# Kernel optimization log

Measured on AMD Instinct MI355X. Metric: run time of the kernel, lower is better.

## Reference

```python
import jax, jax.numpy as jnp
import numpy as np

NUM_FIELDS = 40
EMBED_DIM = 128
BATCH = 1024
NUM_IX = NUM_FIELDS * (NUM_FIELDS - 1) // 2  # 780


def _pair_indices(num_fields):
    row, col = [], []
    for i in range(num_fields - 1):
        for j in range(i + 1, num_fields):
            row.append(i)
            col.append(j)
    return np.asarray(row, dtype=np.int32), np.asarray(col, dtype=np.int32)


def setup_inputs() -> dict:
    key = jax.random.key(0)
    k1, k2 = jax.random.split(key)
    x = jax.random.normal(k1, (BATCH, NUM_FIELDS, EMBED_DIM), dtype=jnp.float32)
    # 'mat' kernel: (embed_dim, num_ix, embed_dim), random_normal init
    kernel = jax.random.normal(k2, (EMBED_DIM, NUM_IX, EMBED_DIM), dtype=jnp.float32) * 0.05
    return {"x": x, "kernel": kernel}


def reference(x, kernel) -> jnp.ndarray:
    # x: (B, F, D); kernel: (D, num_ix, D)
    row, col = _pair_indices(x.shape[1])
    p = x[:, row, :]  # (B, num_ix, D)
    q = x[:, col, :]  # (B, num_ix, D)
    # Original: tmp[b,e,n] = sum_d p[b,n,d]*kernel[e,n,d]; kp[b,n] = sum_e tmp[b,e,n]*q[b,n,e]
    # Fused contraction, never materializing the (B, D, num_ix, D) tensor:
    kp = jnp.einsum('bnd,end,bne->bn', p, kernel, q)
    return kp  # (B, num_ix)
```

## Files before the change

### kernel.cpp

```cpp
#include <hip/hip_runtime.h>

#define NF 40
#define ED 128
#define NB 1024
#define NIX 780
#define XROW (NF * ED)
#define KROW (NIX * ED)
#define XB_BYTES (NB * NF * ED * 2)
#define KB_BYTES (NIX * ED * ED * 2)
#define WS_NEED (XB_BYTES + KB_BYTES)

typedef __attribute__((ext_vector_type(8))) short bf16x8;
typedef __attribute__((ext_vector_type(4))) float f32x4;
typedef __attribute__((ext_vector_type(4))) unsigned short ushx4;
typedef __attribute__((ext_vector_type(8))) unsigned short ushx8;

__device__ __forceinline__ unsigned short f2bf(float x) {
  unsigned int u = __float_as_uint(x);
  u = (u + 0x7FFFu + ((u >> 16) & 1u)) >> 16;
  return (unsigned short)u;
}
__device__ __forceinline__ float bf2f(unsigned short h) {
  return __uint_as_float(((unsigned int)h) << 16);
}

#define GLOAD16(gsrc, ldst)                                                    \
  __builtin_amdgcn_global_load_lds(                                            \
      (const __attribute__((address_space(1))) void*)(gsrc),                   \
      (__attribute__((address_space(3))) void*)(ldst), 16, 0, 0)

__global__ void cvt_fused(const float* __restrict__ x, const float* __restrict__ kr,
                          unsigned short* __restrict__ xb, unsigned short* __restrict__ kb) {
  const int blk = blockIdx.x;
  if (blk < 2560) {
    const size_t g = ((size_t)blk * 256 + threadIdx.x) * 8;
    float4 a = *reinterpret_cast<const float4*>(x + g);
    float4 b = *reinterpret_cast<const float4*>(x + g + 4);
    ushx8 h;
    h[0] = f2bf(a.x); h[1] = f2bf(a.y); h[2] = f2bf(a.z); h[3] = f2bf(a.w);
    h[4] = f2bf(b.x); h[5] = f2bf(b.y); h[6] = f2bf(b.z); h[7] = f2bf(b.w);
    *reinterpret_cast<ushx8*>(xb + g) = h;
  } else {
    const size_t g = ((size_t)(blk - 2560) * 256 + threadIdx.x) * 4;
    const int d = (int)(g & 127);
    const size_t t = g >> 7;
    const int e = (int)(t & 127);
    const int n = (int)(t >> 7);
    float4 v = *reinterpret_cast<const float4*>(kr + ((size_t)e * NIX + n) * ED + d);
    ushx4 h;
    h[0] = f2bf(v.x); h[1] = f2bf(v.y); h[2] = f2bf(v.z); h[3] = f2bf(v.w);
    *reinterpret_cast<ushx4*>(kb + g) = h;
  }
}

__launch_bounds__(256, 4)
__global__ void opn_ws(const unsigned short* __restrict__ xb,
                       const unsigned short* __restrict__ kb,
                       float* __restrict__ out) {
  __shared__ unsigned short S[16384];
  __shared__ float scratch[4][32];

  const int bid = blockIdx.x;
  const int g8 = bid & 7;
  const int n = ((bid >> 3) << 1) + (g8 & 1);
  const int b0base = (g8 >> 1) * 256;

  const int tid = threadIdx.x;
  const int lane = tid & 63;
  const int w = tid >> 6;
  const int lm = lane & 15;
  const int lq = lane >> 4;
  const int col8 = lm * 8;

  int fi = 0, base = 0;
  while (base + (NF - 1 - fi) <= n) { base += NF - 1 - fi; ++fi; }
  const int fj = fi + 1 + (n - base);

  {
    const unsigned short* ks = kb + (size_t)n * (ED * ED);
    #pragma unroll
    for (int j = 0; j < 8; ++j) {
      const int chunk = j * 4 + w;
      const int r = chunk * 4 + lq;
      const int c = col8 ^ ((r & 7) << 3);
      GLOAD16(ks + r * ED + c, S + chunk * 512);
    }
  }
  __syncthreads();

  bf16x8 afr[4][2];
  #pragma unroll
  for (int kk = 0; kk < 4; ++kk)
    #pragma unroll
    for (int f = 0; f < 2; ++f) {
      const int r = w * 32 + f * 16 + lm;
      afr[kk][f] = *reinterpret_cast<const bf16x8*>(
          &S[r * ED + ((kk * 32 + lq * 8) ^ ((r & 7) << 3))]);
    }
  #pragma unroll
  for (int kk = 0; kk < 4; ++kk)
    #pragma unroll
    for (int f = 0; f < 2; ++f)
      asm volatile("" : "+v"(afr[kk][f]));
  __syncthreads();

  unsigned short* Plds = S;
  unsigned short* Qlds = S + 4096;

  #pragma unroll 1
  for (int t = 0; t < 8; ++t) {
    const int b0 = b0base + t * 32;

    #pragma unroll
    for (int j = 0; j < 2; ++j) {
      const int chunk = j * 4 + w;
      const int r = chunk * 4 + lq;
      const int c = col8 ^ ((r & 7) << 3);
      const size_t xoff = (size_t)(b0 + r) * XROW + c;
      GLOAD16(xb + xoff + (size_t)fi * ED, Plds + chunk * 512);
      GLOAD16(xb + xoff + (size_t)fj * ED, Qlds + chunk * 512);
    }
    __syncthreads();

    f32x4 acc[2][2];
    #pragma unroll
    for (int f = 0; f < 2; ++f)
      #pragma unroll
      for (int nt = 0; nt < 2; ++nt)
        acc[f][nt] = (f32x4){0.f, 0.f, 0.f, 0.f};

    __builtin_amdgcn_s_setprio(1);
    #pragma unroll
    for (int kk = 0; kk < 4; ++kk) {
      #pragma unroll
      for (int nt = 0; nt < 2; ++nt) {
        const int pb = nt * 16 + lm;
        bf16x8 pfr = *reinterpret_cast<const bf16x8*>(
            &Plds[pb * ED + ((kk * 32 + lq * 8) ^ ((pb & 7) << 3))]);
        #pragma unroll
        for (int f = 0; f < 2; ++f)
          acc[f][nt] = __builtin_amdgcn_mfma_f32_16x16x32_bf16(afr[kk][f], pfr, acc[f][nt], 0, 0, 0);
      }
    }
    __builtin_amdgcn_s_setprio(0);

    float s[2];
    #pragma unroll
    for (int nt = 0; nt < 2; ++nt) {
      const int qrow = nt * 16 + lm;
      float t0 = 0.f, t1 = 0.f, t2 = 0.f, t3 = 0.f;
      #pragma unroll
      for (int f = 0; f < 2; ++f) {
        const int c = (w * 32 + f * 16 + lq * 4) ^ ((qrow & 7) << 3);
        ushx4 q4 = *reinterpret_cast<const ushx4*>(&Qlds[qrow * ED + c]);
        t0 = fmaf(acc[f][nt][0], bf2f(q4[0]), t0);
        t1 = fmaf(acc[f][nt][1], bf2f(q4[1]), t1);
        t2 = fmaf(acc[f][nt][2], bf2f(q4[2]), t2);
        t3 = fmaf(acc[f][nt][3], bf2f(q4[3]), t3);
      }
      float sv = (t0 + t1) + (t2 + t3);
      sv += __shfl_xor(sv, 16);
      sv += __shfl_xor(sv, 32);
      s[nt] = sv;
    }
    if (lq == 0) {
      scratch[w][lm] = s[0];
      scratch[w][16 + lm] = s[1];
    }
    __syncthreads();

    if (tid < 32) {
      const int b = tid;
      float r = (scratch[0][b] + scratch[1][b]) + (scratch[2][b] + scratch[3][b]);
      out[(size_t)(b0 + b) * NIX + n] = r;
    }
  }
}

__device__ __forceinline__ int swz_fb(int row, int col) {
  return row * 128 + (col ^ ((row & 7) << 3));
}

__launch_bounds__(256, 2)
__global__ void opn_fb(const float* __restrict__ x,
                       const float* __restrict__ kern,
                       float* __restrict__ out) {
  __shared__ unsigned short Klds[128 * 128];
  __shared__ unsigned short Plds[64 * 128];
  __shared__ unsigned short Qlds[64 * 132];

  const int n = blockIdx.x;
  const int tid = threadIdx.x;
  const int lane = tid & 63;
  const int w = tid >> 6;
  const int lm = lane & 15;
  const int lq = lane >> 4;

  int fi = 0, base = 0;
  while (base + (NF - 1 - fi) <= n) { base += NF - 1 - fi; ++fi; }
  const int fj = fi + 1 + (n - base);

  {
    const int r8 = tid >> 5;
    const int d0 = (tid & 31) * 4;
    const float* kbp = kern + (size_t)n * ED + d0;
    #pragma unroll
    for (int p = 0; p < 16; ++p) {
      int e = p * 8 + r8;
      float4 v = *reinterpret_cast<const float4*>(kbp + (size_t)e * KROW);
      ushx4 h;
      h[0] = f2bf(v.x); h[1] = f2bf(v.y); h[2] = f2bf(v.z); h[3] = f2bf(v.w);
      *reinterpret_cast<ushx4*>(&Klds[swz_fb(e, d0)]) = h;
    }
  }
  __syncthreads();

  bf16x8 bfr[4][8];
  #pragma unroll
  for (int kk = 0; kk < 4; ++kk)
    #pragma unroll
    for (int f = 0; f < 8; ++f)
      bfr[kk][f] = *reinterpret_cast<const bf16x8*>(
          &Klds[swz_fb(f * 16 + lm, kk * 32 + lq * 8)]);

  const int r8 = tid >> 5;
  const int c4 = (tid & 31) * 4;

  for (int t = 0; t < 8; ++t) {
    const int b0 = blockIdx.y * 512 + t * 64;
    __syncthreads();
    #pragma unroll
    for (int p = 0; p < 8; ++p) {
      int r = p * 8 + r8;
      const float* xbp = x + (size_t)(b0 + r) * XROW + c4;
      float4 vp = *reinterpret_cast<const float4*>(xbp + fi * ED);
      ushx4 hp;
      hp[0] = f2bf(vp.x); hp[1] = f2bf(vp.y); hp[2] = f2bf(vp.z); hp[3] = f2bf(vp.w);
      *reinterpret_cast<ushx4*>(&Plds[swz_fb(r, c4)]) = hp;
      float4 vq = *reinterpret_cast<const float4*>(xbp + fj * ED);
      ushx4 hq;
      hq[0] = f2bf(vq.x); hq[1] = f2bf(vq.y); hq[2] = f2bf(vq.z); hq[3] = f2bf(vq.w);
      *reinterpret_cast<ushx4*>(&Qlds[r * 132 + c4]) = hq;
    }
    __syncthreads();

    f32x4 acc[8];
    #pragma unroll
    for (int f = 0; f < 8; ++f) acc[f] = (f32x4){0.f, 0.f, 0.f, 0.f};
    #pragma unroll
    for (int kk = 0; kk < 4; ++kk) {
      bf16x8 a = *reinterpret_cast<const bf16x8*>(
          &Plds[swz_fb(w * 16 + lm, kk * 32 + lq * 8)]);
      #pragma unroll
      for (int f = 0; f < 8; ++f)
        acc[f] = __builtin_amdgcn_mfma_f32_16x16x32_bf16(a, bfr[kk][f], acc[f], 0, 0, 0);
    }

    #pragma unroll
    for (int r = 0; r < 4; ++r) {
      const int bl = w * 16 + lq * 4 + r;
      float s = 0.f;
      #pragma unroll
      for (int f = 0; f < 8; ++f)
        s = fmaf(acc[f][r], bf2f(Qlds[bl * 132 + f * 16 + lm]), s);
      s += __shfl_xor(s, 1);
      s += __shfl_xor(s, 2);
      s += __shfl_xor(s, 4);
      s += __shfl_xor(s, 8);
      if (lm == 0) out[(size_t)(b0 + bl) * NIX + n] = s;
    }
  }
}

extern "C" void kernel_launch(void* const* d_in, const int* in_sizes, int n_in,
                              void* d_out, int out_size, void* d_ws, size_t ws_size,
                              hipStream_t stream) {
  const float* x = (const float*)d_in[0];
  const float* kern = (const float*)d_in[1];
  float* out = (float*)d_out;
  (void)in_sizes; (void)n_in; (void)out_size;

  if (ws_size >= (size_t)WS_NEED) {
    unsigned short* xb = (unsigned short*)d_ws;
    unsigned short* kbuf = (unsigned short*)((char*)d_ws + XB_BYTES);
    cvt_fused<<<15040, 256, 0, stream>>>(x, kern, xb, kbuf);
    opn_ws<<<3120, 256, 0, stream>>>(xb, kbuf, out);
  } else {
    dim3 grid(NIX, 2, 1);
    opn_fb<<<grid, 256, 0, stream>>>(x, kern, out);
  }
}
```

Measured before the change: 70.30 us.

## Double-buffer P/Q tiles in LDS and defer cross-wave reduction to kernel end

Splits the shared buffer into two halves so the global-to-LDS load of the next batch tile is issued while the current tile runs its MFMA and Q-dot work. Per-iteration partial sums stay in registers, and the shuffle, scratch write and cross-wave sum happen once after the loop, so one barrier per iteration goes away. This reuses the LDS space previously freed after the A-fragment load. The costs are more live registers (16 result floats, fully unrolled loop) and a larger scratch array, which may pressure the 4-blocks-per-SM occupancy target.

Result: slower. 127.9 us (+82.0%).

```diff
diff --git a/kernel.cpp b/kernel.cpp
--- a/kernel.cpp
+++ b/kernel.cpp
@@ -58,7 +58,7 @@
                        const unsigned short* __restrict__ kb,
                        float* __restrict__ out) {
   __shared__ unsigned short S[16384];
-  __shared__ float scratch[4][32];
+  __shared__ float scratchF[1024];
 
   const int bid = blockIdx.x;
   const int g8 = bid & 7;
@@ -104,23 +104,35 @@
       asm volatile("" : "+v"(afr[kk][f]));
   __syncthreads();
 
-  unsigned short* Plds = S;
-  unsigned short* Qlds = S + 4096;
-
-  #pragma unroll 1
-  for (int t = 0; t < 8; ++t) {
+  unsigned short* bufA = S;
+  unsigned short* bufB = S + 8192;
+
+  auto stage = [&](unsigned short* buf, int t) {
     const int b0 = b0base + t * 32;
-
     #pragma unroll
     for (int j = 0; j < 2; ++j) {
       const int chunk = j * 4 + w;
       const int r = chunk * 4 + lq;
       const int c = col8 ^ ((r & 7) << 3);
       const size_t xoff = (size_t)(b0 + r) * XROW + c;
-      GLOAD16(xb + xoff + (size_t)fi * ED, Plds + chunk * 512);
-      GLOAD16(xb + xoff + (size_t)fj * ED, Qlds + chunk * 512);
-    }
-    __syncthreads();
+      GLOAD16(xb + xoff + (size_t)fi * ED, buf + chunk * 512);
+      GLOAD16(xb + xoff + (size_t)fj * ED, buf + 4096 + chunk * 512);
+    }
+  };
+
+  float res[8][2];
+
+  stage(bufA, 0);
+  __syncthreads();
+
+  #pragma unroll
+  for (int t = 0; t < 8; ++t) {
+    unsigned short* cur = (t & 1) ? bufB : bufA;
+    unsigned short* nxt = (t & 1) ? bufA : bufB;
+    if (t + 1 < 8) stage(nxt, t + 1);
+
+    const unsigned short* Pl = cur;
+    const unsigned short* Ql = cur + 4096;
 
     f32x4 acc[2][2];
     #pragma unroll
@@ -136,7 +148,7 @@
       for (int nt = 0; nt < 2; ++nt) {
         const int pb = nt * 16 + lm;
         bf16x8 pfr = *reinterpret_cast<const bf16x8*>(
-            &Plds[pb * ED + ((kk * 32 + lq * 8) ^ ((pb & 7) << 3))]);
+            &Pl[pb * ED + ((kk * 32 + lq * 8) ^ ((pb & 7) << 3))]);
         #pragma unroll
         for (int f = 0; f < 2; ++f)
           acc[f][nt] = __builtin_amdgcn_mfma_f32_16x16x32_bf16(afr[kk][f], pfr, acc[f][nt], 0, 0, 0);
@@ -144,7 +156,6 @@
     }
     __builtin_amdgcn_s_setprio(0);
 
-    float s[2];
     #pragma unroll
     for (int nt = 0; nt < 2; ++nt) {
       const int qrow = nt * 16 + lm;
@@ -152,28 +163,33 @@
       #pragma unroll
       for (int f = 0; f < 2; ++f) {
         const int c = (w * 32 + f * 16 + lq * 4) ^ ((qrow & 7) << 3);
-        ushx4 q4 = *reinterpret_cast<const ushx4*>(&Qlds[qrow * ED + c]);
+        ushx4 q4 = *reinterpret_cast<const ushx4*>(&Ql[qrow * ED + c]);
         t0 = fmaf(acc[f][nt][0], bf2f(q4[0]), t0);
         t1 = fmaf(acc[f][nt][1], bf2f(q4[1]), t1);
         t2 = fmaf(acc[f][nt][2], bf2f(q4[2]), t2);
         t3 = fmaf(acc[f][nt][3], bf2f(q4[3]), t3);
       }
-      float sv = (t0 + t1) + (t2 + t3);
+      res[t][nt] = (t0 + t1) + (t2 + t3);
+    }
+    __syncthreads();
+  }
+
+  #pragma unroll
+  for (int t = 0; t < 8; ++t)
+    #pragma unroll
+    for (int nt = 0; nt < 2; ++nt) {
+      float sv = res[t][nt];
       sv += __shfl_xor(sv, 16);
       sv += __shfl_xor(sv, 32);
-      s[nt] = sv;
-    }
-    if (lq == 0) {
-      scratch[w][lm] = s[0];
-      scratch[w][16 + lm] = s[1];
-    }
-    __syncthreads();
-
-    if (tid < 32) {
-      const int b = tid;
-      float r = (scratch[0][b] + scratch[1][b]) + (scratch[2][b] + scratch[3][b]);
-      out[(size_t)(b0 + b) * NIX + n] = r;
-    }
+      if (lq == 0) scratchF[(w * 8 + t) * 32 + nt * 16 + lm] = sv;
+    }
+  __syncthreads();
+  {
+    const int t = tid >> 5;
+    const int b = tid & 31;
+    const float v = (scratchF[(0 * 8 + t) * 32 + b] + scratchF[(1 * 8 + t) * 32 + b]) +
+                    (scratchF[(2 * 8 + t) * 32 + b] + scratchF[(3 * 8 + t) * 32 + b]);
+    out[(size_t)(b0base + t * 32 + b) * NIX + n] = v;
   }
 }
 
```

## Group field pairs into 2x2 blocks to reuse x tiles across four interactions

Applied to the files above, without the earlier changes.

Each block now handles a 2x2 group of field pairs (or one diagonal pair for the 20 same-group cases) across 512 threads. The four pair kernels are hoisted into registers, and each loaded P/Q row tile is shared by four interactions, cutting x traffic from global memory. The grid shrinks from 3120 to 840 blocks and K staging becomes four serialized load/sync phases. The trade-offs are higher register pressure, which risks lower occupancy, and uneven work between the 4-pair and 1-pair blocks.

New measurement: 103.9 us. 47.7% more time.

```diff
diff --git a/kernel.cpp b/kernel.cpp
--- a/kernel.cpp
+++ b/kernel.cpp
@@ -22,6 +22,9 @@
 }
 __device__ __forceinline__ float bf2f(unsigned short h) {
   return __uint_as_float(((unsigned int)h) << 16);
+}
+__device__ __forceinline__ int nix_of(int i, int j) {
+  return i * (2 * NF - i - 1) / 2 + (j - i - 1);
 }
 
 #define GLOAD16(gsrc, ldst)                                                    \
@@ -53,17 +56,17 @@
   }
 }
 
-__launch_bounds__(256, 4)
+__launch_bounds__(512, 4)
 __global__ void opn_ws(const unsigned short* __restrict__ xb,
                        const unsigned short* __restrict__ kb,
                        float* __restrict__ out) {
   __shared__ unsigned short S[16384];
-  __shared__ float scratch[4][32];
+  __shared__ float scratchF[8 * 4 * 32];
 
   const int bid = blockIdx.x;
-  const int g8 = bid & 7;
-  const int n = ((bid >> 3) << 1) + (g8 & 1);
-  const int b0base = (g8 >> 1) * 256;
+  const int slice = bid & 3;
+  const int wi = bid >> 2;
+  const int b0base = slice * 256;
 
   const int tid = threadIdx.x;
   const int lane = tid & 63;
@@ -72,107 +75,132 @@
   const int lq = lane >> 4;
   const int col8 = lm * 8;
 
-  int fi = 0, base = 0;
-  while (base + (NF - 1 - fi) <= n) { base += NF - 1 - fi; ++fi; }
-  const int fj = fi + 1 + (n - base);
-
-  {
+  int fA0, fB0, npairs;
+  if (wi < 190) {
+    int ca = 0, base = 0;
+    while (base + (19 - ca) <= wi) { base += 19 - ca; ++ca; }
+    const int cb = ca + 1 + (wi - base);
+    fA0 = 2 * ca; fB0 = 2 * cb; npairs = 4;
+  } else {
+    const int c = wi - 190;
+    fA0 = 2 * c; fB0 = 2 * c + 1; npairs = 1;
+  }
+
+  bf16x8 kfr0[4], kfr1[4], kfr2[4], kfr3[4];
+
+  auto stageK = [&](int n) {
     const unsigned short* ks = kb + (size_t)n * (ED * ED);
     #pragma unroll
-    for (int j = 0; j < 8; ++j) {
-      const int chunk = j * 4 + w;
+    for (int j = 0; j < 4; ++j) {
+      const int chunk = j * 8 + w;
       const int r = chunk * 4 + lq;
       const int c = col8 ^ ((r & 7) << 3);
       GLOAD16(ks + r * ED + c, S + chunk * 512);
     }
-  }
+  };
+  auto hoistK = [&](bf16x8 (&kf)[4]) {
+    const int r = w * 16 + lm;
+    #pragma unroll
+    for (int kk = 0; kk < 4; ++kk)
+      kf[kk] = *reinterpret_cast<const bf16x8*>(
+          &S[r * ED + ((kk * 32 + lq * 8) ^ ((r & 7) << 3))]);
+    #pragma unroll
+    for (int kk = 0; kk < 4; ++kk)
+      asm volatile("" : "+v"(kf[kk]));
+  };
+
+  stageK(nix_of(fA0, fB0));
   __syncthreads();
-
-  bf16x8 afr[4][2];
-  #pragma unroll
-  for (int kk = 0; kk < 4; ++kk)
-    #pragma unroll
-    for (int f = 0; f < 2; ++f) {
-      const int r = w * 32 + f * 16 + lm;
-      afr[kk][f] = *reinterpret_cast<const bf16x8*>(
-          &S[r * ED + ((kk * 32 + lq * 8) ^ ((r & 7) << 3))]);
-    }
-  #pragma unroll
-  for (int kk = 0; kk < 4; ++kk)
-    #pragma unroll
-    for (int f = 0; f < 2; ++f)
-      asm volatile("" : "+v"(afr[kk][f]));
+  hoistK(kfr0);
   __syncthreads();
-
-  unsigned short* Plds = S;
-  unsigned short* Qlds = S + 4096;
+  if (npairs == 4) {
+    stageK(nix_of(fA0, fB0 + 1));
+    __syncthreads();
+    hoistK(kfr1);
+    __syncthreads();
+    stageK(nix_of(fA0 + 1, fB0));
+    __syncthreads();
+    hoistK(kfr2);
+    __syncthreads();
+    stageK(nix_of(fA0 + 1, fB0 + 1));
+    __syncthreads();
+    hoistK(kfr3);
+    __syncthreads();
+  }
+
+
+  auto pair_do = [&](const bf16x8 (&kf)[4], int Poff, int Qoff, int p) {
+    f32x4 acc0 = (f32x4){0.f, 0.f, 0.f, 0.f};
+    f32x4 acc1 = (f32x4){0.f, 0.f, 0.f, 0.f};
+    __builtin_amdgcn_s_setprio(1);
+    #pragma unroll
+    for (int kk = 0; kk < 4; ++kk) {
+      const int cswz = (kk * 32 + lq * 8) ^ ((lm & 7) << 3);
+      bf16x8 pf0 = *reinterpret_cast<const bf16x8*>(&S[Poff + lm * ED + cswz]);
+      acc0 = __builtin_amdgcn_mfma_f32_16x16x32_bf16(kf[kk], pf0, acc0, 0, 0, 0);
+      bf16x8 pf1 = *reinterpret_cast<const bf16x8*>(&S[Poff + (16 + lm) * ED + cswz]);
+      acc1 = __builtin_amdgcn_mfma_f32_16x16x32_bf16(kf[kk], pf1, acc1, 0, 0, 0);
+    }
+    __builtin_amdgcn_s_setprio(0);
+    const int cq = (w * 16 + lq * 4) ^ ((lm & 7) << 3);
+    {
+      const int qrow = lm;
+      ushx4 q4 = *reinterpret_cast<const ushx4*>(&S[Qoff + qrow * ED + cq]);
+      float sv = fmaf(acc0[0], bf2f(q4[0]),
+                 fmaf(acc0[1], bf2f(q4[1]),
+                 fmaf(acc0[2], bf2f(q4[2]), acc0[3] * bf2f(q4[3]))));
+      sv += __shfl_xor(sv, 16);
+      sv += __shfl_xor(sv, 32);
+      if (lq == 0) scratchF[(w * 4 + p) * 32 + qrow] = sv;
+    }
+    {
+      const int qrow = 16 + lm;
+      ushx4 q4 = *reinterpret_cast<const ushx4*>(&S[Qoff + qrow * ED + cq]);
+      float sv = fmaf(acc1[0], bf2f(q4[0]),
+                 fmaf(acc1[1], bf2f(q4[1]),
+                 fmaf(acc1[2], bf2f(q4[2]), acc1[3] * bf2f(q4[3]))));
+      sv += __shfl_xor(sv, 16);
+      sv += __shfl_xor(sv, 32);
+      if (lq == 0) scratchF[(w * 4 + p) * 32 + qrow] = sv;
+    }
+  };
 
   #pragma unroll 1
   for (int t = 0; t < 8; ++t) {
     const int b0 = b0base + t * 32;
 
-    #pragma unroll
-    for (int j = 0; j < 2; ++j) {
-      const int chunk = j * 4 + w;
-      const int r = chunk * 4 + lq;
+    {
+      const int r = w * 4 + lq;
       const int c = col8 ^ ((r & 7) << 3);
       const size_t xoff = (size_t)(b0 + r) * XROW + c;
-      GLOAD16(xb + xoff + (size_t)fi * ED, Plds + chunk * 512);
-      GLOAD16(xb + xoff + (size_t)fj * ED, Qlds + chunk * 512);
-    }
-    __syncthreads();
-
-    f32x4 acc[2][2];
-    #pragma unroll
-    for (int f = 0; f < 2; ++f)
+      const int dst = w * 512 + lane * 8;
+      GLOAD16(xb + xoff + (size_t)fA0 * ED, S + dst);
+      GLOAD16(xb + xoff + (size_t)fB0 * ED, S + 8192 + dst);
+      if (npairs == 4) {
+        GLOAD16(xb + xoff + (size_t)(fA0 + 1) * ED, S + 4096 + dst);
+        GLOAD16(xb + xoff + (size_t)(fB0 + 1) * ED, S + 12288 + dst);
+      }
+    }
+    __syncthreads();
+
+    pair_do(kfr0, 0, 8192, 0);
+    if (npairs == 4) {
+      pair_do(kfr1, 0, 12288, 1);
+      pair_do(kfr2, 4096, 8192, 2);
+      pair_do(kfr3, 4096, 12288, 3);
+    }
+    __syncthreads();
+
+    if (tid < 32 * npairs) {
+      const int p = tid >> 5;
+      const int b = tid & 31;
+      float v = 0.f;
       #pragma unroll
-      for (int nt = 0; nt < 2; ++nt)
-        acc[f][nt] = (f32x4){0.f, 0.f, 0.f, 0.f};
-
-    __builtin_amdgcn_s_setprio(1);
-    #pragma unroll
-    for (int kk = 0; kk < 4; ++kk) {
-      #pragma unroll
-      for (int nt = 0; nt < 2; ++nt) {
-        const int pb = nt * 16 + lm;
-        bf16x8 pfr = *reinterpret_cast<const bf16x8*>(
-            &Plds[pb * ED + ((kk * 32 + lq * 8) ^ ((pb & 7) << 3))]);
-        #pragma unroll
-        for (int f = 0; f < 2; ++f)
-          acc[f][nt] = __builtin_amdgcn_mfma_f32_16x16x32_bf16(afr[kk][f], pfr, acc[f][nt], 0, 0, 0);
-      }
-    }
-    __builtin_amdgcn_s_setprio(0);
-
-    float s[2];
-    #pragma unroll
-    for (int nt = 0; nt < 2; ++nt) {
-      const int qrow = nt * 16 + lm;
-      float t0 = 0.f, t1 = 0.f, t2 = 0.f, t3 = 0.f;
-      #pragma unroll
-      for (int f = 0; f < 2; ++f) {
-        const int c = (w * 32 + f * 16 + lq * 4) ^ ((qrow & 7) << 3);
-        ushx4 q4 = *reinterpret_cast<const ushx4*>(&Qlds[qrow * ED + c]);
-        t0 = fmaf(acc[f][nt][0], bf2f(q4[0]), t0);
-        t1 = fmaf(acc[f][nt][1], bf2f(q4[1]), t1);
-        t2 = fmaf(acc[f][nt][2], bf2f(q4[2]), t2);
-        t3 = fmaf(acc[f][nt][3], bf2f(q4[3]), t3);
-      }
-      float sv = (t0 + t1) + (t2 + t3);
-      sv += __shfl_xor(sv, 16);
-      sv += __shfl_xor(sv, 32);
-      s[nt] = sv;
-    }
-    if (lq == 0) {
-      scratch[w][lm] = s[0];
-      scratch[w][16 + lm] = s[1];
-    }
-    __syncthreads();
-
-    if (tid < 32) {
-      const int b = tid;
-      float r = (scratch[0][b] + scratch[1][b]) + (scratch[2][b] + scratch[3][b]);
-      out[(size_t)(b0 + b) * NIX + n] = r;
+      for (int w8 = 0; w8 < 8; ++w8)
+        v += scratchF[(w8 * 4 + p) * 32 + b];
+      const int fi = fA0 + (p >> 1);
+      const int fj = fB0 + (p & 1);
+      out[(size_t)(b0 + b) * NIX + nix_of(fi, fj)] = v;
     }
   }
 }
@@ -284,7 +312,7 @@
     unsigned short* xb = (unsigned short*)d_ws;
     unsigned short* kbuf = (unsigned short*)((char*)d_ws + XB_BYTES);
     cvt_fused<<<15040, 256, 0, stream>>>(x, kern, xb, kbuf);
-    opn_ws<<<3120, 256, 0, stream>>>(xb, kbuf, out);
+    opn_ws<<<840, 512, 0, stream>>>(xb, kbuf, out);
   } else {
     dim3 grid(NIX, 2, 1);
     opn_fb<<<grid, 256, 0, stream>>>(x, kern, out);
```
